# Kernel tuning notes

Measured on AMD Instinct MI355X. Metric: run time of the kernel, lower is better.

Reference implementation:

```python
import jax, jax.numpy as jnp
import numpy as np

N = 50000      # nodes
E = 400000     # edges
H = 64         # hidden_dim
HEADS = 4
OUT = 64       # out_channels per head (concat=False -> mean over heads)
R = 4          # num_relations
EA = 16        # edge_attr_dim
REL = 8        # rel_emb_dim
ED = EA + REL  # GATv2 edge_dim
FFN = 128      # int(hidden_dim * ffn_ratio)
GRID = 5
ORDER = 3
K = GRID + ORDER          # 8 spline bases
GPTS = GRID + 2*ORDER + 1 # 12 extended grid points
EPS_LN = 1e-5


def make_grid(in_features):
    h_step = 2.0 / GRID  # grid_range (-1, 1)
    g = jnp.arange(-ORDER, GRID + ORDER + 1, dtype=jnp.float32) * h_step - 1.0
    return jnp.tile(g, (in_features, 1))  # [in, GPTS]


def setup_inputs() -> dict:
    key = jax.random.key(0)
    ks = jax.random.split(key, 24)
    s = 0.1
    inp = {
        "h": jax.random.normal(ks[0], (N, H), jnp.float32),
        "edge_index": jax.random.randint(ks[1], (2, E), 0, N, dtype=jnp.int64),
        "edge_attr": jax.random.normal(ks[2], (E, EA), jnp.float32),
        "edge_type": jax.random.randint(ks[3], (E,), 0, R, dtype=jnp.int64),
        # per-relation GATv2 parameters (stacked over relations)
        "rel_emb": jax.random.normal(ks[4], (R, REL), jnp.float32) * s,
        "rel_gate": jax.random.normal(ks[5], (R,), jnp.float32) * s,
        "Wl": jax.random.normal(ks[6], (R, H, HEADS*OUT), jnp.float32) * s,
        "bl": jnp.zeros((R, HEADS*OUT), jnp.float32),
        "Wr": jax.random.normal(ks[7], (R, H, HEADS*OUT), jnp.float32) * s,
        "br": jnp.zeros((R, HEADS*OUT), jnp.float32),
        "We": jax.random.normal(ks[8], (R, ED, HEADS*OUT), jnp.float32) * s,
        "be": jnp.zeros((R, HEADS*OUT), jnp.float32),
        "att": jax.random.normal(ks[9], (R, HEADS, OUT), jnp.float32) * s,
        "out_bias": jnp.zeros((R, OUT), jnp.float32),
        # LayerNorms
        "ln1_g": jnp.ones((H,), jnp.float32), "ln1_b": jnp.zeros((H,), jnp.float32),
        "ln2_g": jnp.ones((H,), jnp.float32), "ln2_b": jnp.zeros((H,), jnp.float32),
        # KAN layer 1: H -> FFN
        "base_w1": jax.random.normal(ks[10], (FFN, H), jnp.float32) * s,
        "spline_w1": jax.random.normal(ks[11], (FFN, H, K), jnp.float32) * s,
        "scaler1": 1.0 + jax.random.normal(ks[12], (FFN, H), jnp.float32) * s,
        "grid1": make_grid(H),
        # KAN layer 2: FFN -> H
        "base_w2": jax.random.normal(ks[13], (H, FFN), jnp.float32) * s,
        "spline_w2": jax.random.normal(ks[14], (H, FFN, K), jnp.float32) * s,
        "scaler2": 1.0 + jax.random.normal(ks[15], (H, FFN), jnp.float32) * s,
        "grid2": make_grid(FFN),
    }
    return inp


def b_splines(x, grid):
    # x: [n, in], grid: [in, GPTS] -> [n, in, K] (Cox-de Boor recursion)
    xe = x[..., None]
    b = ((xe >= grid[:, :-1]) & (xe < grid[:, 1:])).astype(x.dtype)
    for k in range(1, ORDER + 1):
        b = ((xe - grid[:, : -(k + 1)]) / (grid[:, k:-1] - grid[:, : -(k + 1)]) * b[..., :-1]
             + (grid[:, k + 1:] - xe) / (grid[:, k + 1:] - grid[:, 1:-k]) * b[..., 1:])
    return b


def kan_linear(x, base_w, spline_w, scaler, grid):
    base = jax.nn.silu(x) @ base_w.T
    sb = b_splines(x, grid)               # [n, in, K]
    sw = spline_w * scaler[..., None]     # [out, in, K]
    return base + jnp.einsum('nik,oik->no', sb, sw)


def layer_norm(x, g, b):
    mu = x.mean(-1, keepdims=True)
    var = ((x - mu) ** 2).mean(-1, keepdims=True)
    return (x - mu) * jax.lax.rsqrt(var + EPS_LN) * g + b


def gatv2_relation(h, src, dst, ea_full, mask, Wl, bl, Wr, br, We, be, att, ob):
    xl = (h @ Wl + bl).reshape(N, HEADS, OUT)   # lin_l(x) -> source transform
    xr = (h @ Wr + br).reshape(N, HEADS, OUT)   # lin_r(x) -> target transform
    e = (ea_full @ We + be).reshape(-1, HEADS, OUT)
    z = jax.nn.leaky_relu(xl[src] + xr[dst] + e, 0.2)   # [E, heads, out]
    logits = jnp.einsum('eho,ho->eh', z, att)
    neg = jnp.finfo(logits.dtype).min
    logits = jnp.where(mask[:, None], logits, neg)
    # segment softmax over destination nodes (only edges of this relation)
    m = jax.ops.segment_max(logits, dst, num_segments=N)
    ex = jnp.where(mask[:, None], jnp.exp(logits - m[dst]), 0.0)
    denom = jax.ops.segment_sum(ex, dst, num_segments=N) + 1e-16
    alpha = ex / denom[dst]                              # [E, heads]
    out = jax.ops.segment_sum(xl[src] * alpha[..., None], dst, num_segments=N)
    return out.mean(axis=1) + ob                          # concat=False -> head mean, + bias


def reference(h, edge_index, edge_attr, edge_type, rel_emb, rel_gate,
              Wl, bl, Wr, br, We, be, att, out_bias,
              ln1_g, ln1_b, ln2_g, ln2_b,
              base_w1, spline_w1, scaler1, grid1,
              base_w2, spline_w2, scaler2, grid2):
    src, dst = edge_index[0], edge_index[1]
    gate = jax.nn.softmax(rel_gate)  # all relations assumed active
    h_msg = jnp.zeros_like(h)
    for r in range(R):  # fixed small relation count
        mask = edge_type == r
        ea_full = jnp.concatenate(
            [edge_attr, jnp.broadcast_to(rel_emb[r], (E, REL))], axis=-1)
        h_r = gatv2_relation(h, src, dst, ea_full, mask,
                             Wl[r], bl[r], Wr[r], br[r], We[r], be[r],
                             att[r], out_bias[r])
        h_msg = h_msg + gate[r] * h_r
    x = layer_norm(h + h_msg, ln1_g, ln1_b)
    y = kan_linear(x, base_w1, spline_w1, scaler1, grid1)
    y = kan_linear(y, base_w2, spline_w2, scaler2, grid2)
    return layer_norm(x + y, ln2_g, ln2_b)
```

## Files before the change

### kernel.cpp

```cpp
#include <hip/hip_runtime.h>
#include <math.h>

#define DEV __device__ __forceinline__

constexpr int NN   = 50000;
constexpr int EE   = 400000;
constexpr int NB   = (EE + 255) / 256;

typedef short bf16x8 __attribute__((ext_vector_type(8)));
typedef float f32x4  __attribute__((ext_vector_type(4)));

DEV void atomicMaxF(float* addr, float val) {
    int iv = __float_as_int(val);
    if (iv >= 0) atomicMax((int*)addr, iv);
    else         atomicMin((unsigned int*)addr, __float_as_uint(val));
}

DEV float lrelu(float v) { return v >= 0.f ? v : 0.2f * v; }

DEV unsigned short f2bf(float f) {
    unsigned int u = __float_as_uint(f);
    u = (u + 0x7FFF + ((u >> 16) & 1)) >> 16;
    return (unsigned short)u;
}
DEV unsigned int packbf(float a, float b) {
    return (unsigned int)f2bf(a) | ((unsigned int)f2bf(b) << 16);
}

DEV void splines(float x, const float* gs, const float* invA, const float* invB,
                 float* bb8) {
    float bb[11];
#pragma unroll
    for (int j = 0; j < 11; ++j)
        bb[j] = (x >= gs[j] && x < gs[j + 1]) ? 1.f : 0.f;
#pragma unroll
    for (int k = 1; k <= 3; ++k) {
#pragma unroll
        for (int j = 0; j + k < 11; ++j)
            bb[j] = (x - gs[j]) * invA[(k - 1) * 10 + j] * bb[j] +
                    (gs[j + k + 1] - x) * invB[(k - 1) * 10 + j] * bb[j + 1];
    }
#pragma unroll
    for (int k = 0; k < 8; ++k) bb8[k] = bb[k];
}

__global__ void prep_small(const float* __restrict__ rel_gate,
                           const float* __restrict__ out_bias,
                           const float* __restrict__ rel_emb,
                           const float* __restrict__ We,
                           const float* __restrict__ be,
                           float* __restrict__ gate, float* __restrict__ biasvec,
                           float* __restrict__ ebase) {
    __shared__ float gs[4];
    int tid = threadIdx.x;
    if (tid == 0) {
        float g0 = rel_gate[0], g1 = rel_gate[1], g2 = rel_gate[2], g3 = rel_gate[3];
        float mx = fmaxf(fmaxf(g0, g1), fmaxf(g2, g3));
        float e0 = expf(g0 - mx), e1 = expf(g1 - mx), e2 = expf(g2 - mx), e3 = expf(g3 - mx);
        float s = e0 + e1 + e2 + e3;
        gs[0] = e0 / s; gs[1] = e1 / s; gs[2] = e2 / s; gs[3] = e3 / s;
        gate[0] = gs[0]; gate[1] = gs[1]; gate[2] = gs[2]; gate[3] = gs[3];
    }
    __syncthreads();
    if (tid < 64) {
        float b = 0.f;
        for (int r = 0; r < 4; ++r) b += gs[r] * out_bias[r * 64 + tid];
        biasvec[tid] = b;
    }
    for (int r = 0; r < 4; ++r) {
        float v = be[r * 256 + tid];
        for (int i = 0; i < 8; ++i)
            v += rel_emb[r * 8 + i] * We[((size_t)(r * 24 + 16 + i)) * 256 + tid];
        ebase[r * 256 + tid] = v;
    }
}

__global__ void prep_wpack(const float* __restrict__ bw1, const float* __restrict__ sw1,
                           const float* __restrict__ sc1,
                           const float* __restrict__ bw2, const float* __restrict__ sw2,
                           const float* __restrict__ sc2,
                           unsigned short* __restrict__ P1,
                           unsigned short* __restrict__ P2) {
    const int tot1 = 73728;
    const int tot  = tot1 + 73728;
    for (int idx = blockIdx.x * blockDim.x + threadIdx.x; idx < tot;
         idx += gridDim.x * blockDim.x) {
        bool l2 = idx >= tot1;
        int e = l2 ? idx - tot1 : idx;
        int i = e & 7, lane = (e >> 3) & 63, fi = e >> 9;
        int NF = l2 ? 4 : 8;
        int kb = fi / NF, fb = fi % NF;
        int k = kb * 32 + ((lane >> 4) << 3) + i;
        int f = fb * 16 + (lane & 15);
        float v;
        if (!l2) {
            if (k < 64) v = bw1[f * 64 + k];
            else { int t = k - 64; int ii = t >> 3, j = t & 7;
                   v = sw1[(f * 64 + ii) * 8 + j] * sc1[f * 64 + ii]; }
            P1[e] = f2bf(v);
        } else {
            if (k < 128) v = bw2[f * 128 + k];
            else { int t = k - 128; int ii = t >> 3, j = t & 7;
                   v = sw2[(f * 128 + ii) * 8 + j] * sc2[f * 128 + ii]; }
            P2[e] = f2bf(v);
        }
    }
}

__global__ void prep_wpack_lr(const float* __restrict__ Wl,
                              const float* __restrict__ Wr,
                              unsigned short* __restrict__ PLR) {
    int idx = blockIdx.x * blockDim.x + threadIdx.x;
    if (idx >= 4 * 32768) return;
    int r = idx >> 15, e = idx & 32767;
    int i = e & 7, lane = (e >> 3) & 63, fi = e >> 9;
    int kb = fi >> 5, fb = fi & 31;
    int k = kb * 32 + ((lane >> 4) << 3) + i;
    int f = fb * 16 + (lane & 15);
    float v = (f < 256) ? Wl[((size_t)(r * 64 + k)) * 256 + f]
                        : Wr[((size_t)(r * 64 + k)) * 256 + (f - 256)];
    PLR[idx] = f2bf(v);
}

__global__ void fill_init(float* __restrict__ hmsg, float* __restrict__ m,
                          float* __restrict__ den) {
    const int n1 = NN * 64, n2 = NN * 16;
    const int tot = n1 + n2 + n2;
    for (int i = blockIdx.x * blockDim.x + threadIdx.x; i < tot;
         i += gridDim.x * blockDim.x) {
        if (i < n1) hmsg[i] = 0.f;
        else if (i < n1 + n2) m[i - n1] = -3.402823466e38f;
        else den[i - n1 - n2] = 0.f;
    }
}

__global__ void count_hist(const int* __restrict__ etype, int* __restrict__ bc) {
    __shared__ int lc[4];
    int tid = threadIdx.x;
    if (tid < 4) lc[tid] = 0;
    __syncthreads();
    int e = blockIdx.x * 256 + tid;
    if (e < EE) atomicAdd(&lc[etype[e]], 1);
    __syncthreads();
    if (tid < 4) bc[blockIdx.x * 4 + tid] = lc[tid];
}

__global__ void scan_blocks(const int* __restrict__ bc, int* __restrict__ bbase,
                            int* __restrict__ cnt) {
    int w = threadIdx.x >> 6, lane = threadIdx.x & 63;
    int running = 0;
    for (int b0 = 0; b0 < NB; b0 += 64) {
        int b = b0 + lane;
        int v = (b < NB) ? bc[b * 4 + w] : 0;
        int s = v;
#pragma unroll
        for (int off = 1; off < 64; off <<= 1) {
            int t = __shfl_up(s, off, 64);
            if (lane >= off) s += t;
        }
        if (b < NB) bbase[b * 4 + w] = running + s - v;
        running += __shfl(s, 63, 64);
    }
    if (lane == 0) cnt[w] = running;
}

__global__ void scatter_kernel(const int* __restrict__ etype,
                               const int* __restrict__ bbase,
                               int* __restrict__ eids) {
    __shared__ int lbase[4], lofs[4];
    int tid = threadIdx.x;
    if (tid < 4) { lbase[tid] = bbase[blockIdx.x * 4 + tid]; lofs[tid] = 0; }
    __syncthreads();
    int e = blockIdx.x * 256 + tid;
    if (e < EE) {
        int t = etype[e];
        int p = atomicAdd(&lofs[t], 1);
        eids[t * EE + lbase[t] + p] = e;
    }
}

__global__ __launch_bounds__(256) void gemm_mfma_xlxr(
    const float* __restrict__ hin, const unsigned short* __restrict__ P,
    const float* __restrict__ bl, const float* __restrict__ br,
    float* __restrict__ XL, float* __restrict__ XR) {
    int tid = threadIdx.x, wv = tid >> 6, lane = tid & 63;
    int row0 = blockIdx.x * 32;
    f32x4 acc[2][8];
#pragma unroll
    for (int rf = 0; rf < 2; ++rf)
#pragma unroll
        for (int cf = 0; cf < 8; ++cf) acc[rf][cf] = (f32x4){0.f, 0.f, 0.f, 0.f};
#pragma unroll
    for (int kb = 0; kb < 2; ++kb) {
        bf16x8 a[2];
#pragma unroll
        for (int rf = 0; rf < 2; ++rf) {
            int row = row0 + rf * 16 + (lane & 15);
            int k0 = kb * 32 + ((lane >> 4) << 3);
            bf16x8 av = (bf16x8){0, 0, 0, 0, 0, 0, 0, 0};
            if (row < NN) {
                const float4 f0 = *reinterpret_cast<const float4*>(
                    hin + (size_t)row * 64 + k0);
                const float4 f1 = *reinterpret_cast<const float4*>(
                    hin + (size_t)row * 64 + k0 + 4);
                av[0] = (short)f2bf(f0.x); av[1] = (short)f2bf(f0.y);
                av[2] = (short)f2bf(f0.z); av[3] = (short)f2bf(f0.w);
                av[4] = (short)f2bf(f1.x); av[5] = (short)f2bf(f1.y);
                av[6] = (short)f2bf(f1.z); av[7] = (short)f2bf(f1.w);
            }
            a[rf] = av;
        }
#pragma unroll
        for (int cf = 0; cf < 8; ++cf) {
            int fi = kb * 32 + wv * 8 + cf;
            bf16x8 b = *(const bf16x8*)(P + (((size_t)fi * 64 + lane) << 3));
            acc[0][cf] = __builtin_amdgcn_mfma_f32_16x16x32_bf16(a[0], b, acc[0][cf], 0, 0, 0);
            acc[1][cf] = __builtin_amdgcn_mfma_f32_16x16x32_bf16(a[1], b, acc[1][cf], 0, 0, 0);
        }
    }
#pragma unroll
    for (int cf = 0; cf < 8; ++cf) {
        int fc = (wv * 8 + cf) * 16 + (lane & 15);
        bool left = fc < 256;
        float bias = left ? bl[fc] : br[fc - 256];
        float* base = left ? (XL + fc) : (XR + (fc - 256));
#pragma unroll
        for (int rf = 0; rf < 2; ++rf)
#pragma unroll
            for (int r4 = 0; r4 < 4; ++r4) {
                int grow = row0 + rf * 16 + ((lane >> 4) << 2) + r4;
                if (grow < NN) base[(size_t)grow * 256] = acc[rf][cf][r4] + bias;
            }
    }
}

__global__ void pass1_kernel(const int* __restrict__ eidx, const float* __restrict__ eattr,
                             const int* __restrict__ eids, const int* __restrict__ cnt, int r,
                             const float* __restrict__ We, const float* __restrict__ att,
                             const float* __restrict__ ebase,
                             const float* __restrict__ XL, const float* __restrict__ XR,
                             float* __restrict__ elog, float* __restrict__ mbuf) {
    __shared__ float4 we_s[16 * 64];
    __shared__ float4 att_s[64];
    __shared__ float4 eb_s[64];
    int tid = threadIdx.x;
    for (int i = tid; i < 16 * 256; i += 256) {
        int k = i >> 8, j = i & 255;
        ((float*)we_s)[i] = We[((size_t)(r * 24 + k)) * 256 + j];
    }
    ((float*)att_s)[tid] = att[r * 256 + tid];
    ((float*)eb_s)[tid]  = ebase[r * 256 + tid];
    __syncthreads();
    int cntr = cnt[r];
    int wave = (blockIdx.x << 2) + (tid >> 6);
    int lane = tid & 63;
    int nw = gridDim.x << 2;
    for (int i = wave; i < cntr; i += nw) {
        int e = eids[r * EE + i];
        int src = eidx[e], dst = eidx[EE + e];
        float ea[16];
#pragma unroll
        for (int k = 0; k < 16; ++k) ea[k] = eattr[(size_t)e * 16 + k];
        const float4 xl = *reinterpret_cast<const float4*>(XL + (size_t)src * 256 + lane * 4);
        const float4 xr = *reinterpret_cast<const float4*>(XR + (size_t)dst * 256 + lane * 4);
        float4 ev = eb_s[lane];
#pragma unroll
        for (int k = 0; k < 16; ++k) {
            float4 w = we_s[k * 64 + lane];
            ev.x = fmaf(ea[k], w.x, ev.x);
            ev.y = fmaf(ea[k], w.y, ev.y);
            ev.z = fmaf(ea[k], w.z, ev.z);
            ev.w = fmaf(ea[k], w.w, ev.w);
        }
        float4 z;
        z.x = lrelu(xl.x + xr.x + ev.x);
        z.y = lrelu(xl.y + xr.y + ev.y);
        z.z = lrelu(xl.z + xr.z + ev.z);
        z.w = lrelu(xl.w + xr.w + ev.w);
        float4 a4 = att_s[lane];
        float p = z.x * a4.x + z.y * a4.y + z.z * a4.z + z.w * a4.w;
        p += __shfl_xor(p, 1, 64);
        p += __shfl_xor(p, 2, 64);
        p += __shfl_xor(p, 4, 64);
        p += __shfl_xor(p, 8, 64);
        if ((lane & 15) == 0) {
            int hh = lane >> 4;
            elog[(size_t)e * 4 + hh] = p;
            atomicMaxF(mbuf + ((size_t)r * NN + dst) * 4 + hh, p);
        }
    }
}

__global__ void pass2_kernel(const int* __restrict__ eidx, const int* __restrict__ eids,
                             const int* __restrict__ cnt, int r,
                             float* __restrict__ elog, const float* __restrict__ mbuf,
                             float* __restrict__ den) {
    int cntr = cnt[r];
    int tot = cntr * 4;
    for (int idx = blockIdx.x * blockDim.x + threadIdx.x; idx < tot;
         idx += gridDim.x * blockDim.x) {
        int i = idx >> 2, hh = idx & 3;
        int e = eids[r * EE + i];
        int dst = eidx[EE + e];
        size_t mi = ((size_t)r * NN + dst) * 4 + hh;
        float ex = expf(elog[(size_t)e * 4 + hh] - mbuf[mi]);
        elog[(size_t)e * 4 + hh] = ex;
        atomicAdd(den + mi, ex);
    }
}

__global__ void pass3_kernel(const int* __restrict__ eidx, const int* __restrict__ eids,
                             const int* __restrict__ cnt, int r,
                             const float* __restrict__ elog, const float* __restrict__ den,
                             const float* __restrict__ gate,
                             const float* __restrict__ XL, float* __restrict__ hmsg) {
    int cntr = cnt[r];
    float coef = 0.25f * gate[r];
    int wave = (blockIdx.x << 2) + (threadIdx.x >> 6);
    int lane = threadIdx.x & 63;
    int nw = gridDim.x << 2;
    for (int i = wave; i < cntr; i += nw) {
        int e = eids[r * EE + i];
        int src = eidx[e], dst = eidx[EE + e];
        size_t mb = ((size_t)r * NN + dst) * 4;
        float a0 = elog[(size_t)e * 4 + 0] / (den[mb + 0] + 1e-16f);
        float a1 = elog[(size_t)e * 4 + 1] / (den[mb + 1] + 1e-16f);
        float a2 = elog[(size_t)e * 4 + 2] / (den[mb + 2] + 1e-16f);
        float a3 = elog[(size_t)e * 4 + 3] / (den[mb + 3] + 1e-16f);
        const float* xlp = XL + (size_t)src * 256;
        float val = a0 * xlp[lane] + a1 * xlp[64 + lane] +
                    a2 * xlp[128 + lane] + a3 * xlp[192 + lane];
        atomicAdd(hmsg + (size_t)dst * 64 + lane, coef * val);
    }
}

__global__ void ln_kernel(const float* __restrict__ a, const float* __restrict__ badd,
                          const float* __restrict__ biasvec,
                          const float* __restrict__ g, const float* __restrict__ b,
                          float* __restrict__ out) {
    int row = blockIdx.x * 4 + (threadIdx.x >> 6);
    int l = threadIdx.x & 63;
    if (row >= NN) return;
    float v = a[(size_t)row * 64 + l] + badd[(size_t)row * 64 + l];
    if (biasvec) v += biasvec[l];
    float s = v;
#pragma unroll
    for (int mm = 1; mm < 64; mm <<= 1) s += __shfl_xor(s, mm, 64);
    float mu = s * (1.f / 64.f);
    float d = v - mu;
    float s2 = d * d;
#pragma unroll
    for (int mm = 1; mm < 64; mm <<= 1) s2 += __shfl_xor(s2, mm, 64);
    float var = s2 * (1.f / 64.f);
    out[(size_t)row * 64 + l] = d * rsqrtf(var + 1e-5f) * g[l] + b[l];
}

template <int IN, int F, int NWF>
__global__ __launch_bounds__(256) void kan_mfma(const float* __restrict__ Xin,
                                                const unsigned short* __restrict__ P,
                                                const float* __restrict__ grid,
                                                float* __restrict__ Yout) {
    constexpr int K  = IN * 9;
    constexpr int KB = K / 32;
    constexpr int RS = K * 2;
    constexpr int NF = F / 16;
    __shared__ __align__(16) unsigned short act[32 * K];
    __shared__ float gs[12];
    __shared__ float invA[30], invB[30];
    int tid = threadIdx.x;
    if (tid < 12) gs[tid] = grid[tid];
    __syncthreads();
    if (tid < 30) {
        int k = tid / 10 + 1, j = tid % 10;
        if (j + k < 11) {
            invA[tid] = 1.f / (gs[j + k] - gs[j]);
            invB[tid] = 1.f / (gs[j + k + 1] - gs[j + 1]);
        }
    }
    __syncthreads();
    int row0 = blockIdx.x * 32;
    constexpr int PER = 32 * IN / 256;
#pragma unroll
    for (int p = 0; p < PER; ++p) {
        int flat = p * 256 + tid;
        int row = flat / IN, i = flat % IN;
        int n = row0 + row;
        float x = (n < NN) ? Xin[(size_t)n * IN + i] : 0.f;
        float sig = 1.f / (1.f + expf(-x));
        float bb[8];
        splines(x, gs, invA, invB, bb);
        char* rowp = (char*)act + row * RS;
        unsigned int sw = (unsigned int)(row & 7) << 4;
        *(unsigned short*)(rowp + ((i * 2) ^ sw)) = f2bf(x * sig);
        uint4 pk;
        pk.x = packbf(bb[0], bb[1]);
        pk.y = packbf(bb[2], bb[3]);
        pk.z = packbf(bb[4], bb[5]);
        pk.w = packbf(bb[6], bb[7]);
        *(uint4*)(rowp + (((IN + i * 8) * 2) ^ sw)) = pk;
    }
    __syncthreads();
    int wv = tid >> 6, lane = tid & 63;
    f32x4 acc[2][NWF];
#pragma unroll
    for (int rf = 0; rf < 2; ++rf)
#pragma unroll
        for (int cf = 0; cf < NWF; ++cf) acc[rf][cf] = (f32x4){0.f, 0.f, 0.f, 0.f};
    for (int kb = 0; kb < KB; ++kb) {
        bf16x8 a[2];
#pragma unroll
        for (int rf = 0; rf < 2; ++rf) {
            int row = rf * 16 + (lane & 15);
            int o = (kb * 64 + ((lane >> 4) * 16)) ^ ((row & 7) << 4);
            a[rf] = *(const bf16x8*)((char*)act + row * RS + o);
        }
#pragma unroll
        for (int cf = 0; cf < NWF; ++cf) {
            int fi = kb * NF + wv * NWF + cf;
            bf16x8 b = *(const bf16x8*)(P + (((size_t)fi * 64 + lane) << 3));
#pragma unroll
            for (int rf = 0; rf < 2; ++rf)
                acc[rf][cf] = __builtin_amdgcn_mfma_f32_16x16x32_bf16(
                    a[rf], b, acc[rf][cf], 0, 0, 0);
        }
    }
#pragma unroll
    for (int rf = 0; rf < 2; ++rf)
#pragma unroll
        for (int cf = 0; cf < NWF; ++cf)
#pragma unroll
            for (int r4 = 0; r4 < 4; ++r4) {
                int grow = row0 + rf * 16 + ((lane >> 4) * 4) + r4;
                int f = (wv * NWF + cf) * 16 + (lane & 15);
                if (grow < NN) Yout[(size_t)grow * F + f] = acc[rf][cf][r4];
            }
}

extern "C" void kernel_launch(void* const* d_in, const int* in_sizes, int n_in,
                              void* d_out, int out_size, void* d_ws, size_t ws_size,
                              hipStream_t stream) {
    const float* h        = (const float*)d_in[0];
    const int*   eidx     = (const int*)d_in[1];
    const float* eattr    = (const float*)d_in[2];
    const int*   etype    = (const int*)d_in[3];
    const float* rel_emb  = (const float*)d_in[4];
    const float* rel_gate = (const float*)d_in[5];
    const float* Wl       = (const float*)d_in[6];
    const float* bl       = (const float*)d_in[7];
    const float* Wr       = (const float*)d_in[8];
    const float* br       = (const float*)d_in[9];
    const float* We       = (const float*)d_in[10];
    const float* be       = (const float*)d_in[11];
    const float* att      = (const float*)d_in[12];
    const float* out_bias = (const float*)d_in[13];
    const float* ln1_g    = (const float*)d_in[14];
    const float* ln1_b    = (const float*)d_in[15];
    const float* ln2_g    = (const float*)d_in[16];
    const float* ln2_b    = (const float*)d_in[17];
    const float* bw1      = (const float*)d_in[18];
    const float* sw1      = (const float*)d_in[19];
    const float* sc1      = (const float*)d_in[20];
    const float* grid1    = (const float*)d_in[21];
    const float* bw2      = (const float*)d_in[22];
    const float* sw2      = (const float*)d_in[23];
    const float* sc2      = (const float*)d_in[24];
    const float* grid2    = (const float*)d_in[25];
    float* out = (float*)d_out;
    float* W = (float*)d_ws;

    float* XL    = W + 0;
    float* XR    = W + 12800000;
    float* HM    = W + 25600000;
    float* M     = W + 28800000;
    float* DENb  = W + 29600000;
    float* EL    = W + 30400000;
    int*   EIDS  = (int*)(W + 32000000);
    int*   CNT   = (int*)(W + 33600000);
    float* GATE  = W + 33600064;
    float* BIAS  = W + 33600128;
    float* EBASE = W + 33600192;
    unsigned short* P1  = (unsigned short*)(W + 33601216);
    unsigned short* P2  = (unsigned short*)(W + 33638080);
    unsigned short* PLR = (unsigned short*)(W + 33674944);
    float* X  = W + 0;
    float* Y1 = W + 3200000;
    float* Y2 = W + 9600000;
    int* BC = (int*)(W + 12800000);
    int* BB = (int*)(W + 12800000 + 8192);

    prep_small<<<1, 256, 0, stream>>>(rel_gate, out_bias, rel_emb, We, be,
                                      GATE, BIAS, EBASE);
    prep_wpack<<<576, 256, 0, stream>>>(bw1, sw1, sc1, bw2, sw2, sc2, P1, P2);
    prep_wpack_lr<<<512, 256, 0, stream>>>(Wl, Wr, PLR);
    fill_init<<<2048, 256, 0, stream>>>(HM, M, DENb);
    count_hist<<<NB, 256, 0, stream>>>(etype, BC);
    scan_blocks<<<1, 256, 0, stream>>>(BC, BB, CNT);
    scatter_kernel<<<NB, 256, 0, stream>>>(etype, BB, EIDS);

    for (int r = 0; r < 4; ++r) {
        gemm_mfma_xlxr<<<(NN + 31) / 32, 256, 0, stream>>>(
            h, PLR + (size_t)r * 32768, bl + r * 256, br + r * 256, XL, XR);
        pass1_kernel<<<1024, 256, 0, stream>>>(eidx, eattr, EIDS, CNT, r, We, att,
                                               EBASE, XL, XR, EL, M);
        pass2_kernel<<<1024, 256, 0, stream>>>(eidx, EIDS, CNT, r, EL, M, DENb);
        pass3_kernel<<<1024, 256, 0, stream>>>(eidx, EIDS, CNT, r, EL, DENb, GATE,
                                               XL, HM);
    }

    ln_kernel<<<(NN + 3) / 4, 256, 0, stream>>>(h, HM, BIAS, ln1_g, ln1_b, X);
    kan_mfma<64, 128, 2><<<(NN + 31) / 32, 256, 0, stream>>>(X, P1, grid1, Y1);
    kan_mfma<128, 64, 1><<<(NN + 31) / 32, 256, 0, stream>>>(Y1, P2, grid2, Y2);
    ln_kernel<<<(NN + 3) / 4, 256, 0, stream>>>(X, Y2, nullptr, ln2_g, ln2_b, out);
}
```

Before: 776.3 us.

## Store XL/XR in bf16, use closed-form uniform B-splines, chunk KAN LDS

```diff
diff --git a/kernel.cpp b/kernel.cpp
--- a/kernel.cpp
+++ b/kernel.cpp
@@ -23,25 +23,8 @@
     u = (u + 0x7FFF + ((u >> 16) & 1)) >> 16;
     return (unsigned short)u;
 }
-DEV unsigned int packbf(float a, float b) {
-    return (unsigned int)f2bf(a) | ((unsigned int)f2bf(b) << 16);
-}
-
-DEV void splines(float x, const float* gs, const float* invA, const float* invB,
-                 float* bb8) {
-    float bb[11];
-#pragma unroll
-    for (int j = 0; j < 11; ++j)
-        bb[j] = (x >= gs[j] && x < gs[j + 1]) ? 1.f : 0.f;
-#pragma unroll
-    for (int k = 1; k <= 3; ++k) {
-#pragma unroll
-        for (int j = 0; j + k < 11; ++j)
-            bb[j] = (x - gs[j]) * invA[(k - 1) * 10 + j] * bb[j] +
-                    (gs[j + k + 1] - x) * invB[(k - 1) * 10 + j] * bb[j + 1];
-    }
-#pragma unroll
-    for (int k = 0; k < 8; ++k) bb8[k] = bb[k];
+DEV float bf2f(unsigned short u) {
+    return __uint_as_float(((unsigned int)u) << 16);
 }
 
 __global__ void prep_small(const float* __restrict__ rel_gate,
@@ -182,7 +165,7 @@
 __global__ __launch_bounds__(256) void gemm_mfma_xlxr(
     const float* __restrict__ hin, const unsigned short* __restrict__ P,
     const float* __restrict__ bl, const float* __restrict__ br,
-    float* __restrict__ XL, float* __restrict__ XR) {
+    unsigned short* __restrict__ XLb, unsigned short* __restrict__ XRb) {
     int tid = threadIdx.x, wv = tid >> 6, lane = tid & 63;
     int row0 = blockIdx.x * 32;
     f32x4 acc[2][8];
@@ -223,13 +206,14 @@
         int fc = (wv * 8 + cf) * 16 + (lane & 15);
         bool left = fc < 256;
         float bias = left ? bl[fc] : br[fc - 256];
-        float* base = left ? (XL + fc) : (XR + (fc - 256));
+        unsigned short* base = left ? (XLb + fc) : (XRb + (fc - 256));
 #pragma unroll
         for (int rf = 0; rf < 2; ++rf)
 #pragma unroll
             for (int r4 = 0; r4 < 4; ++r4) {
                 int grow = row0 + rf * 16 + ((lane >> 4) << 2) + r4;
-                if (grow < NN) base[(size_t)grow * 256] = acc[rf][cf][r4] + bias;
+                if (grow < NN)
+                    base[(size_t)grow * 256] = f2bf(acc[rf][cf][r4] + bias);
             }
     }
 }
@@ -238,7 +222,8 @@
                              const int* __restrict__ eids, const int* __restrict__ cnt, int r,
                              const float* __restrict__ We, const float* __restrict__ att,
                              const float* __restrict__ ebase,
-                             const float* __restrict__ XL, const float* __restrict__ XR,
+                             const unsigned short* __restrict__ XLb,
+                             const unsigned short* __restrict__ XRb,
                              float* __restrict__ elog, float* __restrict__ mbuf) {
     __shared__ float4 we_s[16 * 64];
     __shared__ float4 att_s[64];
@@ -261,8 +246,10 @@
         float ea[16];
 #pragma unroll
         for (int k = 0; k < 16; ++k) ea[k] = eattr[(size_t)e * 16 + k];
-        const float4 xl = *reinterpret_cast<const float4*>(XL + (size_t)src * 256 + lane * 4);
-        const float4 xr = *reinterpret_cast<const float4*>(XR + (size_t)dst * 256 + lane * 4);
+        const ushort4 xlu = *reinterpret_cast<const ushort4*>(
+            XLb + (size_t)src * 256 + lane * 4);
+        const ushort4 xru = *reinterpret_cast<const ushort4*>(
+            XRb + (size_t)dst * 256 + lane * 4);
         float4 ev = eb_s[lane];
 #pragma unroll
         for (int k = 0; k < 16; ++k) {
@@ -273,10 +260,10 @@
             ev.w = fmaf(ea[k], w.w, ev.w);
         }
         float4 z;
-        z.x = lrelu(xl.x + xr.x + ev.x);
-        z.y = lrelu(xl.y + xr.y + ev.y);
-        z.z = lrelu(xl.z + xr.z + ev.z);
-        z.w = lrelu(xl.w + xr.w + ev.w);
+        z.x = lrelu(bf2f(xlu.x) + bf2f(xru.x) + ev.x);
+        z.y = lrelu(bf2f(xlu.y) + bf2f(xru.y) + ev.y);
+        z.z = lrelu(bf2f(xlu.z) + bf2f(xru.z) + ev.z);
+        z.w = lrelu(bf2f(xlu.w) + bf2f(xru.w) + ev.w);
         float4 a4 = att_s[lane];
         float p = z.x * a4.x + z.y * a4.y + z.z * a4.z + z.w * a4.w;
         p += __shfl_xor(p, 1, 64);
@@ -313,7 +300,8 @@
                              const int* __restrict__ cnt, int r,
                              const float* __restrict__ elog, const float* __restrict__ den,
                              const float* __restrict__ gate,
-                             const float* __restrict__ XL, float* __restrict__ hmsg) {
+                             const unsigned short* __restrict__ XLb,
+                             float* __restrict__ hmsg) {
     int cntr = cnt[r];
     float coef = 0.25f * gate[r];
     int wave = (blockIdx.x << 2) + (threadIdx.x >> 6);
@@ -327,9 +315,9 @@
         float a1 = elog[(size_t)e * 4 + 1] / (den[mb + 1] + 1e-16f);
         float a2 = elog[(size_t)e * 4 + 2] / (den[mb + 2] + 1e-16f);
         float a3 = elog[(size_t)e * 4 + 3] / (den[mb + 3] + 1e-16f);
-        const float* xlp = XL + (size_t)src * 256;
-        float val = a0 * xlp[lane] + a1 * xlp[64 + lane] +
-                    a2 * xlp[128 + lane] + a3 * xlp[192 + lane];
+        const unsigned short* xlp = XLb + (size_t)src * 256;
+        float val = a0 * bf2f(xlp[lane]) + a1 * bf2f(xlp[64 + lane]) +
+                    a2 * bf2f(xlp[128 + lane]) + a3 * bf2f(xlp[192 + lane]);
         atomicAdd(hmsg + (size_t)dst * 64 + lane, coef * val);
     }
 }
@@ -355,73 +343,93 @@
     out[(size_t)row * 64 + l] = d * rsqrtf(var + 1e-5f) * g[l] + b[l];
 }
 
-template <int IN, int F, int NWF>
+template <int IN, int F, int NWF, int NCH>
 __global__ __launch_bounds__(256) void kan_mfma(const float* __restrict__ Xin,
                                                 const unsigned short* __restrict__ P,
                                                 const float* __restrict__ grid,
                                                 float* __restrict__ Yout) {
-    constexpr int K  = IN * 9;
-    constexpr int KB = K / 32;
-    constexpr int RS = K * 2;
-    constexpr int NF = F / 16;
-    __shared__ __align__(16) unsigned short act[32 * K];
-    __shared__ float gs[12];
-    __shared__ float invA[30], invB[30];
+    constexpr int ICH = IN / NCH;
+    constexpr int KC  = ICH * 9;
+    constexpr int RS  = KC * 2;
+    constexpr int NF  = F / 16;
+    constexpr int SKB = ICH / 32;
+    constexpr int PKB = ICH * 8 / 32;
+    __shared__ __align__(16) unsigned short act[32 * KC];
+    __shared__ float gp[2];
     int tid = threadIdx.x;
-    if (tid < 12) gs[tid] = grid[tid];
+    if (tid == 0) {
+        float g0 = grid[0];
+        gp[0] = g0;
+        gp[1] = 1.f / (grid[1] - g0);
+    }
     __syncthreads();
-    if (tid < 30) {
-        int k = tid / 10 + 1, j = tid % 10;
-        if (j + k < 11) {
-            invA[tid] = 1.f / (gs[j + k] - gs[j]);
-            invB[tid] = 1.f / (gs[j + k + 1] - gs[j + 1]);
-        }
-    }
-    __syncthreads();
+    float g0 = gp[0], invh = gp[1];
     int row0 = blockIdx.x * 32;
-    constexpr int PER = 32 * IN / 256;
-#pragma unroll
-    for (int p = 0; p < PER; ++p) {
-        int flat = p * 256 + tid;
-        int row = flat / IN, i = flat % IN;
-        int n = row0 + row;
-        float x = (n < NN) ? Xin[(size_t)n * IN + i] : 0.f;
-        float sig = 1.f / (1.f + expf(-x));
-        float bb[8];
-        splines(x, gs, invA, invB, bb);
-        char* rowp = (char*)act + row * RS;
-        unsigned int sw = (unsigned int)(row & 7) << 4;
-        *(unsigned short*)(rowp + ((i * 2) ^ sw)) = f2bf(x * sig);
-        uint4 pk;
-        pk.x = packbf(bb[0], bb[1]);
-        pk.y = packbf(bb[2], bb[3]);
-        pk.z = packbf(bb[4], bb[5]);
-        pk.w = packbf(bb[6], bb[7]);
-        *(uint4*)(rowp + (((IN + i * 8) * 2) ^ sw)) = pk;
-    }
-    __syncthreads();
     int wv = tid >> 6, lane = tid & 63;
     f32x4 acc[2][NWF];
 #pragma unroll
     for (int rf = 0; rf < 2; ++rf)
 #pragma unroll
         for (int cf = 0; cf < NWF; ++cf) acc[rf][cf] = (f32x4){0.f, 0.f, 0.f, 0.f};
-    for (int kb = 0; kb < KB; ++kb) {
-        bf16x8 a[2];
-#pragma unroll
-        for (int rf = 0; rf < 2; ++rf) {
-            int row = rf * 16 + (lane & 15);
-            int o = (kb * 64 + ((lane >> 4) * 16)) ^ ((row & 7) << 4);
-            a[rf] = *(const bf16x8*)((char*)act + row * RS + o);
-        }
-#pragma unroll
-        for (int cf = 0; cf < NWF; ++cf) {
-            int fi = kb * NF + wv * NWF + cf;
-            bf16x8 b = *(const bf16x8*)(P + (((size_t)fi * 64 + lane) << 3));
-#pragma unroll
-            for (int rf = 0; rf < 2; ++rf)
-                acc[rf][cf] = __builtin_amdgcn_mfma_f32_16x16x32_bf16(
-                    a[rf], b, acc[rf][cf], 0, 0, 0);
+
+    for (int c = 0; c < NCH; ++c) {
+        if (c > 0) __syncthreads();
+        constexpr int PER = 32 * ICH / 256;
+#pragma unroll
+        for (int p = 0; p < PER; ++p) {
+            int flat = p * 256 + tid;
+            int row = flat / ICH, i = flat % ICH;
+            int n = row0 + row;
+            float x = (n < NN) ? Xin[(size_t)n * IN + c * ICH + i] : 0.f;
+            float sig = 1.f / (1.f + expf(-x));
+            char* rowp = (char*)act + row * RS;
+            unsigned int sw = (unsigned int)(row & 7) << 4;
+            *(unsigned short*)(rowp + ((i * 2) ^ sw)) = f2bf(x * sig);
+            int sb = (ICH + i * 8) * 2;
+            *(uint4*)(rowp + (sb ^ sw)) = (uint4){0u, 0u, 0u, 0u};
+            float pos = (x - g0) * invh;
+            float jf = floorf(pos);
+            int j = (int)jf;
+            float u = pos - jf;
+            if (j >= 0 && j <= 10) {
+                float u2 = u * u, u3 = u2 * u;
+                float om = 1.f - u;
+                const float s6 = 1.f / 6.f;
+                float v0 = u3 * s6;
+                float v1 = (-3.f * u3 + 3.f * u2 + 3.f * u + 1.f) * s6;
+                float v2 = (3.f * u3 - 6.f * u2 + 4.f) * s6;
+                float v3 = om * om * om * s6;
+                if (j < 8)
+                    *(unsigned short*)(rowp + ((sb + j * 2) ^ sw)) = f2bf(v0);
+                if (j >= 1 && j <= 8)
+                    *(unsigned short*)(rowp + ((sb + (j - 1) * 2) ^ sw)) = f2bf(v1);
+                if (j >= 2 && j <= 9)
+                    *(unsigned short*)(rowp + ((sb + (j - 2) * 2) ^ sw)) = f2bf(v2);
+                if (j >= 3)
+                    *(unsigned short*)(rowp + ((sb + (j - 3) * 2) ^ sw)) = f2bf(v3);
+            }
+        }
+        __syncthreads();
+        constexpr int KBC = KC / 32;
+        for (int kbl = 0; kbl < KBC; ++kbl) {
+            int gkb = (kbl < SKB) ? (c * SKB + kbl)
+                                  : (IN / 32 + c * PKB + (kbl - SKB));
+            bf16x8 a[2];
+#pragma unroll
+            for (int rf = 0; rf < 2; ++rf) {
+                int row = rf * 16 + (lane & 15);
+                int o = (kbl * 64 + ((lane >> 4) * 16)) ^ ((row & 7) << 4);
+                a[rf] = *(const bf16x8*)((char*)act + row * RS + o);
+            }
+#pragma unroll
+            for (int cf = 0; cf < NWF; ++cf) {
+                int fi = gkb * NF + wv * NWF + cf;
+                bf16x8 b = *(const bf16x8*)(P + (((size_t)fi * 64 + lane) << 3));
+#pragma unroll
+                for (int rf = 0; rf < 2; ++rf)
+                    acc[rf][cf] = __builtin_amdgcn_mfma_f32_16x16x32_bf16(
+                        a[rf], b, acc[rf][cf], 0, 0, 0);
+            }
         }
     }
 #pragma unroll
@@ -468,8 +476,8 @@
     float* out = (float*)d_out;
     float* W = (float*)d_ws;
 
-    float* XL    = W + 0;
-    float* XR    = W + 12800000;
+    unsigned short* XLb = (unsigned short*)(W + 0);
+    unsigned short* XRb = (unsigned short*)(W + 12800000);
     float* HM    = W + 25600000;
     float* M     = W + 28800000;
     float* DENb  = W + 29600000;
@@ -499,16 +507,16 @@
 
     for (int r = 0; r < 4; ++r) {
         gemm_mfma_xlxr<<<(NN + 31) / 32, 256, 0, stream>>>(
-            h, PLR + (size_t)r * 32768, bl + r * 256, br + r * 256, XL, XR);
+            h, PLR + (size_t)r * 32768, bl + r * 256, br + r * 256, XLb, XRb);
         pass1_kernel<<<1024, 256, 0, stream>>>(eidx, eattr, EIDS, CNT, r, We, att,
-                                               EBASE, XL, XR, EL, M);
+                                               EBASE, XLb, XRb, EL, M);
         pass2_kernel<<<1024, 256, 0, stream>>>(eidx, EIDS, CNT, r, EL, M, DENb);
         pass3_kernel<<<1024, 256, 0, stream>>>(eidx, EIDS, CNT, r, EL, DENb, GATE,
-                                               XL, HM);
+                                               XLb, HM);
     }
 
     ln_kernel<<<(NN + 3) / 4, 256, 0, stream>>>(h, HM, BIAS, ln1_g, ln1_b, X);
-    kan_mfma<64, 128, 2><<<(NN + 31) / 32, 256, 0, stream>>>(X, P1, grid1, Y1);
-    kan_mfma<128, 64, 1><<<(NN + 31) / 32, 256, 0, stream>>>(Y1, P2, grid2, Y2);
+    kan_mfma<64, 128, 2, 1><<<(NN + 31) / 32, 256, 0, stream>>>(X, P1, grid1, Y1);
+    kan_mfma<128, 64, 1, 2><<<(NN + 31) / 32, 256, 0, stream>>>(Y1, P2, grid2, Y2);
     ln_kernel<<<(NN + 3) / 4, 256, 0, stream>>>(X, Y2, nullptr, ln2_g, ln2_b, out);
 }
```

After: 694.9 us. -10.5%, faster.
